# Performance work log

Measured on AMD Instinct MI355X. Metric: run time of the kernel, lower is better.

## Reference

```python
import jax, jax.numpy as jnp
import numpy as np

B, S, H = 1, 2048, 2880
NH, NKV, HD = 64, 8, 64
WIN = 128
ROPE_BASE = 10000.0


def setup_inputs() -> dict:
    key = jax.random.key(0)
    ks = jax.random.split(key, 8)

    def lin(k, fi, fo):
        return (jax.random.normal(k, (fi, fo), jnp.float32) / np.sqrt(fi)).astype(jnp.float32)

    hidden_states = jax.random.normal(ks[0], (B, S, H), jnp.float32)
    Wq = lin(ks[1], H, NH * HD)
    Wk = lin(ks[2], H, NKV * HD)
    Wv = lin(ks[3], H, NKV * HD)
    Wo = lin(ks[4], NH * HD, H)
    bq = jnp.zeros((NH * HD,), jnp.float32)
    bk = jnp.zeros((NKV * HD,), jnp.float32)
    bv = jnp.zeros((NKV * HD,), jnp.float32)
    bo = jnp.zeros((H,), jnp.float32)
    sinks = jax.random.normal(ks[5], (NH,), jnp.float32) * 0.5

    # RoPE tables, shape [B, S, HD] (rotate_half convention: halves duplicated)
    pos = jnp.arange(S, dtype=jnp.float32)
    inv_freq = 1.0 / (ROPE_BASE ** (jnp.arange(0, HD, 2, dtype=jnp.float32) / HD))
    freqs = pos[:, None] * inv_freq[None, :]          # [S, HD/2]
    emb = jnp.concatenate([freqs, freqs], axis=-1)    # [S, HD]
    cos = jnp.broadcast_to(jnp.cos(emb)[None], (B, S, HD))
    sin = jnp.broadcast_to(jnp.sin(emb)[None], (B, S, HD))

    return dict(hidden_states=hidden_states, cos=cos, sin=sin,
                Wq=Wq, bq=bq, Wk=Wk, bk=bk, Wv=Wv, bv=bv, Wo=Wo, bo=bo,
                sinks=sinks, window=WIN)


def _rotate_half(x):
    x1, x2 = jnp.split(x, 2, axis=-1)
    return jnp.concatenate([-x2, x1], axis=-1)


def reference(hidden_states, cos, sin, Wq, bq, Wk, bk, Wv, bv, Wo, bo, sinks, window):
    b, s, _ = hidden_states.shape
    nh = sinks.shape[0]
    hd = Wq.shape[1] // nh
    nkv = Wk.shape[1] // hd
    scale = hd ** -0.5

    q = (hidden_states @ Wq + bq).reshape(b, s, nh, hd)
    k = (hidden_states @ Wk + bk).reshape(b, s, nkv, hd)
    v = (hidden_states @ Wv + bv).reshape(b, s, nkv, hd)

    c = cos[:, :, None, :]  # [b, s, 1, hd]
    sn = sin[:, :, None, :]
    q = q * c + _rotate_half(q) * sn
    k = k * c + _rotate_half(k) * sn

    # GQA: expand kv heads to query heads
    g = nh // nkv
    k_rep = jnp.repeat(k, g, axis=2)  # [b, s, nh, hd]
    v_rep = jnp.repeat(v, g, axis=2)

    scores = jnp.einsum('bqhd,bkhd->bhqk', q, k_rep) * scale  # [b, nh, s, s]

    # causal sliding-window mask
    qi = jnp.arange(s)[:, None]
    ki = jnp.arange(s)[None, :]
    allowed = (qi >= ki) & (qi - ki < window)
    neg = jnp.finfo(scores.dtype).min
    scores = jnp.where(allowed[None, None], scores, neg)

    # virtual sink column at kv index s: score replaced by learned per-head bias
    sink_col = jnp.broadcast_to(sinks[None, :, None, None], (b, nh, s, 1))
    scores = jnp.concatenate([scores, sink_col], axis=-1)  # [b, nh, s, s+1]

    probs = jax.nn.softmax(scores, axis=-1)
    # sink value vector is zeros, so only real columns contribute
    out = jnp.einsum('bhqk,bkhd->bqhd', probs[..., :s], v_rep)
    out = out.reshape(b, s, nh * hd) @ Wo + bo
    return out
```

## Files before the change

### kernel.cpp

```cpp
#include <hip/hip_runtime.h>
#include <stdint.h>
#include <stddef.h>

typedef unsigned short u16;
typedef unsigned int u32;
typedef float f32x4 __attribute__((ext_vector_type(4)));
typedef __bf16 bf16x8 __attribute__((ext_vector_type(8)));
typedef uint32_t u32x4 __attribute__((ext_vector_type(4)));
typedef uint32_t u32x2 __attribute__((ext_vector_type(2)));

#define DEVINL static __device__ __forceinline__
#define VMW(n) asm volatile("s_waitcnt vmcnt(" #n ")" ::: "memory")
#define LGK0() asm volatile("s_waitcnt lgkmcnt(0)" ::: "memory")
#define SB0() __builtin_amdgcn_sched_barrier(0)

DEVINL u16 f2bf(float f) {
  union { float f; u32 u; } x; x.f = f;
  u32 r = (x.u + 0x7fffu + ((x.u >> 16) & 1u)) >> 16;
  return (u16)r;
}
DEVINL float bflo(u32 x) { union { u32 u; float f; } t; t.u = x << 16; return t.f; }
DEVINL float bfhi(u32 x) { union { u32 u; float f; } t; t.u = x & 0xffff0000u; return t.f; }

DEVINL void gl_lds16(const u16* g, u16* l) {
  __builtin_amdgcn_global_load_lds(
      (const __attribute__((address_space(1))) u32*)(const void*)g,
      (__attribute__((address_space(3))) u32*)(void*)l, 16, 0, 0);
}

DEVINL f32x4 mfma16(bf16x8 a, bf16x8 b, f32x4 c) {
  return __builtin_amdgcn_mfma_f32_16x16x32_bf16(a, b, c, 0, 0, 0);
}

DEVINL void rope8(u32x4& v1, u32x4& v2, const float* pc, const float* ps) {
  f32x4 c0 = *(const f32x4*)pc, c1 = *(const f32x4*)(pc + 4);
  f32x4 s0 = *(const f32x4*)ps, s1 = *(const f32x4*)(ps + 4);
  float C[8] = {c0[0], c0[1], c0[2], c0[3], c1[0], c1[1], c1[2], c1[3]};
  float Sn[8] = {s0[0], s0[1], s0[2], s0[3], s1[0], s1[1], s1[2], s1[3]};
  u32x4 r1, r2;
#pragma unroll
  for (int i = 0; i < 4; ++i) {
    float x1l = bflo(v1[i]), x1h = bfhi(v1[i]);
    float x2l = bflo(v2[i]), x2h = bfhi(v2[i]);
    float o1l = x1l * C[2 * i] - x2l * Sn[2 * i];
    float o1h = x1h * C[2 * i + 1] - x2h * Sn[2 * i + 1];
    float o2l = x2l * C[2 * i] + x1l * Sn[2 * i];
    float o2h = x2h * C[2 * i + 1] + x1h * Sn[2 * i + 1];
    r1[i] = (u32)f2bf(o1l) | ((u32)f2bf(o1h) << 16);
    r2[i] = (u32)f2bf(o2l) | ((u32)f2bf(o2h) << 16);
  }
  v1 = r1; v2 = r2;
}

__global__ __launch_bounds__(256) void k_pre(
    const float* __restrict__ hs, u16* __restrict__ hsb,
    const float* __restrict__ Wq, const float* __restrict__ Wk,
    const float* __restrict__ Wv, const float* __restrict__ Wo,
    u16* __restrict__ WqkvT, u16* __restrict__ WoT)
{
  __shared__ float t[64][65];
  int id = blockIdx.x;
  const int tid = threadIdx.x;
  if (id < 5760) {
    int i = id * 256 + tid;
    f32x4 v = ((const f32x4*)hs)[i];
    u32x2 o;
    o[0] = (u32)f2bf(v[0]) | ((u32)f2bf(v[1]) << 16);
    o[1] = (u32)f2bf(v[2]) | ((u32)f2bf(v[3]) << 16);
    ((u32x2*)hsb)[i] = o;
    return;
  }
  id -= 5760;
  const float* src; u16* dst; int R, C, bx, by;
  if (id < 2880)       { src = Wq; dst = WqkvT;                         R = 2880; C = 4096; bx = id & 63; by = id >> 6; }
  else if (id < 3240)  { id -= 2880; src = Wk; dst = WqkvT + (size_t)4096 * 2880; R = 2880; C = 512;  bx = id & 7;  by = id >> 3; }
  else if (id < 3600)  { id -= 3240; src = Wv; dst = WqkvT + (size_t)4608 * 2880; R = 2880; C = 512;  bx = id & 7;  by = id >> 3; }
  else                 { id -= 3600; src = Wo; dst = WoT;               R = 4096; C = 2880; bx = id % 45; by = id / 45; }
  const int r0 = by * 64, c0 = bx * 64;
  {
    const int rr = tid >> 2, cg = (tid & 3) * 16;
    const float* s = src + (size_t)(r0 + rr) * C + c0 + cg;
#pragma unroll
    for (int i = 0; i < 4; ++i) {
      f32x4 v = *(const f32x4*)(s + 4 * i);
      t[rr][cg + 4 * i + 0] = v[0];
      t[rr][cg + 4 * i + 1] = v[1];
      t[rr][cg + 4 * i + 2] = v[2];
      t[rr][cg + 4 * i + 3] = v[3];
    }
  }
  __syncthreads();
  {
    const int rg = tid & 7, cb = tid >> 3;
#pragma unroll
    for (int it = 0; it < 2; ++it) {
      const int c = cb + it * 32;
      float v[8];
#pragma unroll
      for (int i = 0; i < 8; ++i) v[i] = t[rg * 8 + i][c];
      u32x4 o;
#pragma unroll
      for (int j = 0; j < 4; ++j)
        o[j] = (u32)f2bf(v[2 * j]) | ((u32)f2bf(v[2 * j + 1]) << 16);
      *(u32x4*)(dst + (size_t)(c0 + c) * R + r0 + rg * 8) = o;
    }
  }
}

__global__ __launch_bounds__(256, 2) void k_gemmq(
    const u16* __restrict__ A, const u16* __restrict__ Bgl, u16* __restrict__ Cout,
    const float* __restrict__ pb0, const float* __restrict__ pb1, const float* __restrict__ pb2)
{
  constexpr int K = 2880, NT = 45, LDC = 5120;
  __shared__ u16 Asm[2][128 * 64];
  __shared__ u16 Bsm[2][160 * 64];

  const int bid = blockIdx.x;
  const int swz = (bid & 7) * 64 + (bid >> 3);
  const int bx = swz >> 4, by = swz & 15;
  const int m0 = by * 128, n0 = bx * 160;

  const int tid = threadIdx.x;
  const int w = tid >> 6, lane = tid & 63;
  const int l15 = lane & 15, lg = lane >> 4;
  const int wr = w >> 1, wc = w & 1;

  const u16* Ag = A + (size_t)m0 * K;
  const u16* Bg = Bgl + (size_t)n0 * K;

  auto ld1 = [&](const u16* s, u16* d, int slot) {
    int row = slot >> 3, c = slot & 7;
    gl_lds16(s + (size_t)row * K + ((c ^ (row & 7)) << 3), d + row * 64 + c * 8);
  };
  auto stApart = [&](int tg, int part) {
    u16* d = Asm[tg & 1];
    const u16* s = Ag + tg * 64;
    ld1(s, d, part * 256 + tid);
    ld1(s, d, part * 256 + 512 + tid);
  };
  auto stBa = [&](int tg) {
    u16* d = Bsm[tg & 1];
    const u16* s = Bg + tg * 64;
    ld1(s, d, tid);
    ld1(s, d, 640 + tid);
  };
  auto stBb = [&](int tg) {
    u16* d = Bsm[tg & 1];
    const u16* s = Bg + tg * 64;
    ld1(s, d, 256 + tid);
    ld1(s, d, (tid < 128) ? (512 + tid) : (768 + tid));
    ld1(s, d, 1024 + tid);
  };

  const int ra = wr * 64 + l15;
  const int rb = wc * 80 + l15;
  const int x0 = (lg ^ (l15 & 7)) << 3;
  const int x1 = x0 ^ 32;

  f32x4 acc[4][5] = {};
  bf16x8 af[2][2], bfr[5][2];

  stBa(0); stBb(0); stApart(0, 0); stApart(0, 1);
  VMW(2);
  __builtin_amdgcn_s_barrier();
  SB0();

  for (int t = 0; t < NT; ++t) {
    const u16* Ab = Asm[t & 1];
    const u16* Bb_ = Bsm[t & 1];
    const bool st = (t + 1 < NT);
#pragma unroll
    for (int m = 0; m < 2; ++m) {
      af[m][0] = *(const bf16x8*)&Ab[(ra + m * 16) * 64 + x0];
      af[m][1] = *(const bf16x8*)&Ab[(ra + m * 16) * 64 + x1];
    }
#pragma unroll
    for (int n = 0; n < 2; ++n) {
      bfr[n][0] = *(const bf16x8*)&Bb_[(rb + n * 16) * 64 + x0];
      bfr[n][1] = *(const bf16x8*)&Bb_[(rb + n * 16) * 64 + x1];
    }
    if (st) stBa(t + 1);
    LGK0(); SB0();
    __builtin_amdgcn_s_setprio(1);
#pragma unroll
    for (int kk = 0; kk < 2; ++kk)
#pragma unroll
      for (int m = 0; m < 2; ++m)
#pragma unroll
        for (int n = 0; n < 2; ++n)
          acc[m][n] = mfma16(af[m][kk], bfr[n][kk], acc[m][n]);
    __builtin_amdgcn_s_setprio(0);
#pragma unroll
    for (int n = 2; n < 5; ++n) {
      bfr[n][0] = *(const bf16x8*)&Bb_[(rb + n * 16) * 64 + x0];
      bfr[n][1] = *(const bf16x8*)&Bb_[(rb + n * 16) * 64 + x1];
    }
    if (st) stBb(t + 1);
    LGK0(); SB0();
    __builtin_amdgcn_s_setprio(1);
#pragma unroll
    for (int kk = 0; kk < 2; ++kk)
#pragma unroll
      for (int m = 0; m < 2; ++m)
#pragma unroll
        for (int n = 2; n < 5; ++n)
          acc[m][n] = mfma16(af[m][kk], bfr[n][kk], acc[m][n]);
    __builtin_amdgcn_s_setprio(0);
    if (st) { VMW(5); } else { VMW(0); }
    __builtin_amdgcn_s_barrier();
    SB0();
#pragma unroll
    for (int m = 0; m < 2; ++m) {
      af[m][0] = *(const bf16x8*)&Ab[(ra + 32 + m * 16) * 64 + x0];
      af[m][1] = *(const bf16x8*)&Ab[(ra + 32 + m * 16) * 64 + x1];
    }
    if (st) stApart(t + 1, 0);
    LGK0(); SB0();
    __builtin_amdgcn_s_setprio(1);
#pragma unroll
    for (int kk = 0; kk < 2; ++kk)
#pragma unroll
      for (int m = 0; m < 2; ++m)
#pragma unroll
        for (int n = 0; n < 2; ++n)
          acc[2 + m][n] = mfma16(af[m][kk], bfr[n][kk], acc[2 + m][n]);
    __builtin_amdgcn_s_setprio(0);
    if (st) stApart(t + 1, 1);
    __builtin_amdgcn_s_setprio(1);
#pragma unroll
    for (int kk = 0; kk < 2; ++kk)
#pragma unroll
      for (int m = 0; m < 2; ++m)
#pragma unroll
        for (int n = 2; n < 5; ++n)
          acc[2 + m][n] = mfma16(af[m][kk], bfr[n][kk], acc[2 + m][n]);
    __builtin_amdgcn_s_setprio(0);
    VMW(2);
    __builtin_amdgcn_s_barrier();
    SB0();
  }

#pragma unroll
  for (int m2 = 0; m2 < 4; ++m2)
#pragma unroll
    for (int n = 0; n < 5; ++n) {
      int col = n0 + wc * 80 + n * 16 + l15;
      float bias = (col < 4096) ? pb0[col] : (col < 4608) ? pb1[col - 4096] : pb2[col - 4608];
#pragma unroll
      for (int q = 0; q < 4; ++q) {
        int row = m0 + wr * 64 + m2 * 16 + lg * 4 + q;
        Cout[(size_t)row * LDC + col] = f2bf(acc[m2][n][q] + bias);
      }
    }
}

__global__ __launch_bounds__(256, 2) void k_gemmo(
    const u16* __restrict__ A, const u16* __restrict__ Bgl, float* __restrict__ Cout,
    const float* __restrict__ pb0)
{
  constexpr int K = 4096, NT = 64, LDC = 2880;
  __shared__ u16 Asm[2][128 * 64];
  __shared__ u16 Bsm[2][96 * 64];

  const int bid = blockIdx.x;
  const int swz = (bid & 7) * 60 + (bid >> 3);
  const int bx = swz / 16, by = swz & 15;
  const int m0 = by * 128, n0 = bx * 96;

  const int tid = threadIdx.x;
  const int w = tid >> 6, lane = tid & 63;
  const int l15 = lane & 15, lg = lane >> 4;
  const int wr = w >> 1, wc = w & 1;

  const u16* Ag = A + (size_t)m0 * K;
  const u16* Bg = Bgl + (size_t)n0 * K;

  auto ld1 = [&](const u16* s, u16* d, int slot) {
    int row = slot >> 3, c = slot & 7;
    gl_lds16(s + (size_t)row * K + ((c ^ (row & 7)) << 3), d + row * 64 + c * 8);
  };
  auto stApart = [&](int tg, int part) {
    u16* d = Asm[tg & 1];
    const u16* s = Ag + tg * 64;
    ld1(s, d, part * 256 + tid);
    ld1(s, d, part * 256 + 512 + tid);
  };
  auto stB = [&](int tg) {
    u16* d = Bsm[tg & 1];
    const u16* s = Bg + tg * 64;
    ld1(s, d, tid);
    ld1(s, d, 256 + tid);
    ld1(s, d, 512 + tid);
  };

  const int ra = wr * 64 + l15;
  const int rb = wc * 48 + l15;
  const int x0 = (lg ^ (l15 & 7)) << 3;
  const int x1 = x0 ^ 32;

  f32x4 acc[4][3] = {};
  bf16x8 af[2][2], bfr[3][2];

  stB(0); stApart(0, 0); stApart(0, 1);
  VMW(2);
  __builtin_amdgcn_s_barrier();
  SB0();

  for (int t = 0; t < NT; ++t) {
    const u16* Ab = Asm[t & 1];
    const u16* Bb_ = Bsm[t & 1];
    const bool st = (t + 1 < NT);
#pragma unroll
    for (int m = 0; m < 2; ++m) {
      af[m][0] = *(const bf16x8*)&Ab[(ra + m * 16) * 64 + x0];
      af[m][1] = *(const bf16x8*)&Ab[(ra + m * 16) * 64 + x1];
    }
#pragma unroll
    for (int n = 0; n < 3; ++n) {
      bfr[n][0] = *(const bf16x8*)&Bb_[(rb + n * 16) * 64 + x0];
      bfr[n][1] = *(const bf16x8*)&Bb_[(rb + n * 16) * 64 + x1];
    }
    if (st) { stB(t + 1); stApart(t + 1, 0); }
    LGK0(); SB0();
    __builtin_amdgcn_s_setprio(1);
#pragma unroll
    for (int kk = 0; kk < 2; ++kk)
#pragma unroll
      for (int m = 0; m < 2; ++m)
#pragma unroll
        for (int n = 0; n < 3; ++n)
          acc[m][n] = mfma16(af[m][kk], bfr[n][kk], acc[m][n]);
    __builtin_amdgcn_s_setprio(0);
    if (st) { VMW(5); } else { VMW(0); }
    __builtin_amdgcn_s_barrier();
    SB0();
#pragma unroll
    for (int m = 0; m < 2; ++m) {
      af[m][0] = *(const bf16x8*)&Ab[(ra + 32 + m * 16) * 64 + x0];
      af[m][1] = *(const bf16x8*)&Ab[(ra + 32 + m * 16) * 64 + x1];
    }
    if (st) stApart(t + 1, 1);
    LGK0(); SB0();
    __builtin_amdgcn_s_setprio(1);
#pragma unroll
    for (int kk = 0; kk < 2; ++kk)
#pragma unroll
      for (int m = 0; m < 2; ++m)
#pragma unroll
        for (int n = 0; n < 3; ++n)
          acc[2 + m][n] = mfma16(af[m][kk], bfr[n][kk], acc[2 + m][n]);
    __builtin_amdgcn_s_setprio(0);
    VMW(2);
    __builtin_amdgcn_s_barrier();
    SB0();
  }

#pragma unroll
  for (int m2 = 0; m2 < 4; ++m2)
#pragma unroll
    for (int n = 0; n < 3; ++n) {
      int col = n0 + wc * 48 + n * 16 + l15;
      float bias = pb0[col];
#pragma unroll
      for (int q = 0; q < 4; ++q) {
        int row = m0 + wr * 64 + m2 * 16 + lg * 4 + q;
        Cout[(size_t)row * LDC + col] = acc[m2][n][q] + bias;
      }
    }
}

__global__ __launch_bounds__(512, 1) void k_attn(
    const u16* __restrict__ qkv, const float* __restrict__ sinks,
    const float* __restrict__ cosb, const float* __restrict__ sinb,
    u16* __restrict__ aout)
{
  __shared__ u16 Kl[192 * 64];
  __shared__ u16 Vt[64 * 200];
  __shared__ u16 Pl[8][2][16][40];

  const int qt = blockIdx.x * 64;
  const int kv = blockIdx.y;
  const int tid = threadIdx.x;
  const int w = tid >> 6, lane = tid & 63;
  const int l15 = lane & 15, lg = lane >> 4;

  for (int idx = tid; idx < 192 * 4; idx += 512) {
    int row = idx >> 2, ch = idx & 3;
    int key = qt - 128 + row;
    u32x4 v1 = {0, 0, 0, 0}, v2 = {0, 0, 0, 0};
    if (key >= 0) {
      const u16* p = qkv + (size_t)key * 5120 + 4096 + kv * 64 + ch * 8;
      v1 = *(const u32x4*)p;
      v2 = *(const u32x4*)(p + 32);
      rope8(v1, v2, cosb + (size_t)key * 64 + ch * 8, sinb + (size_t)key * 64 + ch * 8);
    }
    int sw = (row & 7) << 4;
    *(u32x4*)((char*)Kl + row * 128 + ((ch * 16) ^ sw)) = v1;
    *(u32x4*)((char*)Kl + row * 128 + (((ch + 4) * 16) ^ sw)) = v2;
  }
  for (int idx = tid; idx < 192 * 8; idx += 512) {
    int row = idx >> 3, ch = idx & 7;
    int key = qt - 128 + row;
    u32x4 val = {0, 0, 0, 0};
    if (key >= 0) val = *(const u32x4*)(qkv + (size_t)key * 5120 + 4608 + kv * 64 + ch * 8);
    const u16* pv16 = (const u16*)&val;
#pragma unroll
    for (int j = 0; j < 8; ++j) Vt[(ch * 8 + j) * 200 + row] = pv16[j];
  }
  __syncthreads();

  const int h = kv * 8 + w;
  const float sink = sinks[h];

  for (int qs = 0; qs < 2; ++qs) {
    const int qb = qt + qs * 32;
    bf16x8 qf[2][2];
#pragma unroll
    for (int rt = 0; rt < 2; ++rt) {
      const int qrow = qb + rt * 16 + l15;
      const u16* p = qkv + (size_t)qrow * 5120 + h * 64 + lg * 8;
      union { u32x4 u; bf16x8 v; } a, b;
      a.u = *(const u32x4*)p;
      b.u = *(const u32x4*)(p + 32);
      rope8(a.u, b.u, cosb + (size_t)qrow * 64 + lg * 8, sinb + (size_t)qrow * 64 + lg * 8);
      qf[rt][0] = a.v;
      qf[rt][1] = b.v;
    }

    f32x4 S[2][5][2];
#pragma unroll
    for (int kb = 0; kb < 5; ++kb)
#pragma unroll
      for (int hh = 0; hh < 2; ++hh) {
        int krow = qs * 32 + kb * 32 + hh * 16 + l15;
        int sw = (krow & 7) << 4;
        bf16x8 kf0 = *(const bf16x8*)((const char*)Kl + krow * 128 + ((lg * 16) ^ sw));
        bf16x8 kf1 = *(const bf16x8*)((const char*)Kl + krow * 128 + ((64 + lg * 16) ^ sw));
#pragma unroll
        for (int rt = 0; rt < 2; ++rt) {
          f32x4 a = {0.f, 0.f, 0.f, 0.f};
          a = mfma16(qf[rt][0], kf0, a);
          a = mfma16(qf[rt][1], kf1, a);
          S[rt][kb][hh] = a;
        }
      }

    float inv_s[2][4];
#pragma unroll
    for (int rt = 0; rt < 2; ++rt)
#pragma unroll
      for (int r = 0; r < 4; ++r) {
        int q_abs = qb + rt * 16 + lg * 4 + r;
        float m = -1e30f;
#pragma unroll
        for (int kb = 0; kb < 5; ++kb)
#pragma unroll
          for (int hh = 0; hh < 2; ++hh) {
            int k_abs = qb - 128 + kb * 32 + hh * 16 + l15;
            float v = S[rt][kb][hh][r] * 0.125f;
            bool ok = (k_abs >= 0) && (k_abs <= q_abs) && (q_abs - k_abs < 128);
            v = ok ? v : -1e30f;
            S[rt][kb][hh][r] = v;
            m = fmaxf(m, v);
          }
        m = fmaxf(m, __shfl_xor(m, 1, 64));
        m = fmaxf(m, __shfl_xor(m, 2, 64));
        m = fmaxf(m, __shfl_xor(m, 4, 64));
        m = fmaxf(m, __shfl_xor(m, 8, 64));
        m = fmaxf(m, sink);
        float sum = 0.f;
#pragma unroll
        for (int kb = 0; kb < 5; ++kb)
#pragma unroll
          for (int hh = 0; hh < 2; ++hh) {
            float p = __expf(S[rt][kb][hh][r] - m);
            S[rt][kb][hh][r] = p;
            sum += p;
          }
        sum += __shfl_xor(sum, 1, 64);
        sum += __shfl_xor(sum, 2, 64);
        sum += __shfl_xor(sum, 4, 64);
        sum += __shfl_xor(sum, 8, 64);
        inv_s[rt][r] = 1.0f / (sum + __expf(sink - m));
      }

    f32x4 pv[2][4] = {};
#pragma unroll
    for (int kb = 0; kb < 5; ++kb) {
      asm volatile("s_waitcnt lgkmcnt(0)" ::: "memory");
#pragma unroll
      for (int rt = 0; rt < 2; ++rt)
#pragma unroll
        for (int hh = 0; hh < 2; ++hh)
#pragma unroll
          for (int r = 0; r < 4; ++r)
            Pl[w][rt][lg * 4 + r][hh * 16 + l15] = f2bf(S[rt][kb][hh][r] * inv_s[rt][r]);
      asm volatile("s_waitcnt lgkmcnt(0)" ::: "memory");
      __builtin_amdgcn_sched_barrier(0);
      bf16x8 a0 = *(const bf16x8*)&Pl[w][0][l15][lg * 8];
      bf16x8 a1 = *(const bf16x8*)&Pl[w][1][l15][lg * 8];
#pragma unroll
      for (int nt = 0; nt < 4; ++nt) {
        bf16x8 vf = *(const bf16x8*)&Vt[(nt * 16 + l15) * 200 + qs * 32 + kb * 32 + lg * 8];
        pv[0][nt] = mfma16(a0, vf, pv[0][nt]);
        pv[1][nt] = mfma16(a1, vf, pv[1][nt]);
      }
    }

#pragma unroll
    for (int rt = 0; rt < 2; ++rt)
#pragma unroll
      for (int nt = 0; nt < 4; ++nt)
#pragma unroll
        for (int r = 0; r < 4; ++r)
          aout[(size_t)(qb + rt * 16 + lg * 4 + r) * 4096 + h * 64 + nt * 16 + l15] =
              f2bf(pv[rt][nt][r]);
  }
}

extern "C" void kernel_launch(void* const* d_in, const int* in_sizes, int n_in,
                              void* d_out, int out_size, void* d_ws, size_t ws_size,
                              hipStream_t stream) {
  const float* hs    = (const float*)d_in[0];
  const float* cosb  = (const float*)d_in[1];
  const float* sinb  = (const float*)d_in[2];
  const float* Wq    = (const float*)d_in[3];
  const float* bq    = (const float*)d_in[4];
  const float* Wk    = (const float*)d_in[5];
  const float* bk    = (const float*)d_in[6];
  const float* Wv    = (const float*)d_in[7];
  const float* bv    = (const float*)d_in[8];
  const float* Wo    = (const float*)d_in[9];
  const float* bo    = (const float*)d_in[10];
  const float* sinks = (const float*)d_in[11];

  char* ws = (char*)d_ws;
  u16* hsb   = (u16*)ws;  ws += (size_t)2048 * 2880 * 2;
  u16* WqkvT = (u16*)ws;  ws += (size_t)5120 * 2880 * 2;
  u16* WoT   = (u16*)ws;  ws += (size_t)2880 * 4096 * 2;
  u16* QKV   = (u16*)ws;  ws += (size_t)2048 * 5120 * 2;
  u16* AOut  = (u16*)ws;  ws += (size_t)2048 * 4096 * 2;

  k_pre<<<12240, 256, 0, stream>>>(hs, hsb, Wq, Wk, Wv, Wo, WqkvT, WoT);

  k_gemmq<<<512, 256, 0, stream>>>(hsb, WqkvT, QKV, bq, bk, bv);

  k_attn<<<dim3(32, 8), 512, 0, stream>>>(QKV, sinks, cosb, sinb, AOut);

  k_gemmo<<<480, 256, 0, stream>>>(AOut, WoT, (float*)d_out, bo);
}
```

Measured before the change: 167.8 us.

## Fuse Wo fp32-to-bf16 transpose into output GEMM B-tile loading

Removes the separate Wo transpose/convert pass from the preprocessing kernel. The output GEMM now reads Wo directly in fp32 through registers, converts it to bf16 and writes it transposed into LDS, with the pipeline restructured to prefetch the next tile at the top of each iteration. This saves a full write and re-read of the bf16 weight copy, at the cost of strided scalar fp32 global loads and extra register and VALU work inside the GEMM. The attention grid is also flattened and its block order swizzled to improve cache locality.

```diff
diff --git a/kernel.cpp b/kernel.cpp
--- a/kernel.cpp
+++ b/kernel.cpp
@@ -55,8 +55,7 @@
 __global__ __launch_bounds__(256) void k_pre(
     const float* __restrict__ hs, u16* __restrict__ hsb,
     const float* __restrict__ Wq, const float* __restrict__ Wk,
-    const float* __restrict__ Wv, const float* __restrict__ Wo,
-    u16* __restrict__ WqkvT, u16* __restrict__ WoT)
+    const float* __restrict__ Wv, u16* __restrict__ WqkvT)
 {
   __shared__ float t[64][65];
   int id = blockIdx.x;
@@ -72,10 +71,9 @@
   }
   id -= 5760;
   const float* src; u16* dst; int R, C, bx, by;
-  if (id < 2880)       { src = Wq; dst = WqkvT;                         R = 2880; C = 4096; bx = id & 63; by = id >> 6; }
-  else if (id < 3240)  { id -= 2880; src = Wk; dst = WqkvT + (size_t)4096 * 2880; R = 2880; C = 512;  bx = id & 7;  by = id >> 3; }
-  else if (id < 3600)  { id -= 3240; src = Wv; dst = WqkvT + (size_t)4608 * 2880; R = 2880; C = 512;  bx = id & 7;  by = id >> 3; }
-  else                 { id -= 3600; src = Wo; dst = WoT;               R = 4096; C = 2880; bx = id % 45; by = id / 45; }
+  if (id < 2880)       { src = Wq; dst = WqkvT;                               R = 2880; C = 4096; bx = id & 63; by = id >> 6; }
+  else if (id < 3240)  { id -= 2880; src = Wk; dst = WqkvT + (size_t)4096 * 2880; R = 2880; C = 512; bx = id & 7; by = id >> 3; }
+  else                 { id -= 3240; src = Wv; dst = WqkvT + (size_t)4608 * 2880; R = 2880; C = 512; bx = id & 7; by = id >> 3; }
   const int r0 = by * 64, c0 = bx * 64;
   {
     const int rr = tid >> 2, cg = (tid & 3) * 16;
@@ -255,10 +253,10 @@
 }
 
 __global__ __launch_bounds__(256, 2) void k_gemmo(
-    const u16* __restrict__ A, const u16* __restrict__ Bgl, float* __restrict__ Cout,
+    const u16* __restrict__ A, const float* __restrict__ Wo, float* __restrict__ Cout,
     const float* __restrict__ pb0)
 {
-  constexpr int K = 4096, NT = 64, LDC = 2880;
+  constexpr int K = 4096, NT = 64, LDC = 2880, NW = 2880;
   __shared__ u16 Asm[2][128 * 64];
   __shared__ u16 Bsm[2][96 * 64];
 
@@ -273,7 +271,6 @@
   const int wr = w >> 1, wc = w & 1;
 
   const u16* Ag = A + (size_t)m0 * K;
-  const u16* Bg = Bgl + (size_t)n0 * K;
 
   auto ld1 = [&](const u16* s, u16* d, int slot) {
     int row = slot >> 3, c = slot & 7;
@@ -285,12 +282,35 @@
     ld1(s, d, part * 256 + tid);
     ld1(s, d, part * 256 + 512 + tid);
   };
-  auto stB = [&](int tg) {
-    u16* d = Bsm[tg & 1];
-    const u16* s = Bg + tg * 64;
-    ld1(s, d, tid);
-    ld1(s, d, 256 + tid);
-    ld1(s, d, 512 + tid);
+
+  int n_[3], oct_[3], bwoff[3];
+  const float* bp[3];
+#pragma unroll
+  for (int i = 0; i < 3; ++i) {
+    int u = i * 256 + tid;
+    n_[i] = u % 96;
+    oct_[i] = u / 96;
+    bp[i] = Wo + (size_t)oct_[i] * 8 * NW + n0 + n_[i];
+    bwoff[i] = n_[i] * 64 + ((oct_[i] ^ (n_[i] & 7)) << 3);
+  }
+  float rB[3][8];
+  auto loadB = [&](int tg) {
+#pragma unroll
+    for (int i = 0; i < 3; ++i) {
+      const float* p = bp[i] + (size_t)tg * 64 * NW;
+#pragma unroll
+      for (int j = 0; j < 8; ++j) rB[i][j] = p[(size_t)j * NW];
+    }
+  };
+  auto writeB = [&](int buf) {
+#pragma unroll
+    for (int i = 0; i < 3; ++i) {
+      u32x4 o;
+#pragma unroll
+      for (int q = 0; q < 4; ++q)
+        o[q] = (u32)f2bf(rB[i][2 * q]) | ((u32)f2bf(rB[i][2 * q + 1]) << 16);
+      *(u32x4*)(&Bsm[buf][bwoff[i]]) = o;
+    }
   };
 
   const int ra = wr * 64 + l15;
@@ -301,8 +321,12 @@
   f32x4 acc[4][3] = {};
   bf16x8 af[2][2], bfr[3][2];
 
-  stB(0); stApart(0, 0); stApart(0, 1);
-  VMW(2);
+  loadB(0);
+  stApart(0, 0); stApart(0, 1);
+  VMW(4);
+  writeB(0);
+  VMW(0);
+  LGK0();
   __builtin_amdgcn_s_barrier();
   SB0();
 
@@ -310,6 +334,11 @@
     const u16* Ab = Asm[t & 1];
     const u16* Bb_ = Bsm[t & 1];
     const bool st = (t + 1 < NT);
+    if (st) {
+      loadB(t + 1);
+      stApart(t + 1, 0); stApart(t + 1, 1);
+    }
+    SB0();
 #pragma unroll
     for (int m = 0; m < 2; ++m) {
       af[m][0] = *(const bf16x8*)&Ab[(ra + m * 16) * 64 + x0];
@@ -320,7 +349,6 @@
       bfr[n][0] = *(const bf16x8*)&Bb_[(rb + n * 16) * 64 + x0];
       bfr[n][1] = *(const bf16x8*)&Bb_[(rb + n * 16) * 64 + x1];
     }
-    if (st) { stB(t + 1); stApart(t + 1, 0); }
     LGK0(); SB0();
     __builtin_amdgcn_s_setprio(1);
 #pragma unroll
@@ -331,15 +359,11 @@
         for (int n = 0; n < 3; ++n)
           acc[m][n] = mfma16(af[m][kk], bfr[n][kk], acc[m][n]);
     __builtin_amdgcn_s_setprio(0);
-    if (st) { VMW(5); } else { VMW(0); }
-    __builtin_amdgcn_s_barrier();
-    SB0();
 #pragma unroll
     for (int m = 0; m < 2; ++m) {
       af[m][0] = *(const bf16x8*)&Ab[(ra + 32 + m * 16) * 64 + x0];
       af[m][1] = *(const bf16x8*)&Ab[(ra + 32 + m * 16) * 64 + x1];
     }
-    if (st) stApart(t + 1, 1);
     LGK0(); SB0();
     __builtin_amdgcn_s_setprio(1);
 #pragma unroll
@@ -350,7 +374,12 @@
         for (int n = 0; n < 3; ++n)
           acc[2 + m][n] = mfma16(af[m][kk], bfr[n][kk], acc[2 + m][n]);
     __builtin_amdgcn_s_setprio(0);
-    VMW(2);
+    if (st) {
+      VMW(4);
+      writeB((t + 1) & 1);
+      VMW(0);
+      LGK0();
+    }
     __builtin_amdgcn_s_barrier();
     SB0();
   }
@@ -378,8 +407,10 @@
   __shared__ u16 Vt[64 * 200];
   __shared__ u16 Pl[8][2][16][40];
 
-  const int qt = blockIdx.x * 64;
-  const int kv = blockIdx.y;
+  const int bid = blockIdx.x;
+  const int swzb = (bid & 7) * 32 + (bid >> 3);
+  const int qt = (swzb & 31) * 64;
+  const int kv = swzb >> 5;
   const int tid = threadIdx.x;
   const int w = tid >> 6, lane = tid & 63;
   const int l15 = lane & 15, lg = lane >> 4;
@@ -537,15 +568,14 @@
   char* ws = (char*)d_ws;
   u16* hsb   = (u16*)ws;  ws += (size_t)2048 * 2880 * 2;
   u16* WqkvT = (u16*)ws;  ws += (size_t)5120 * 2880 * 2;
-  u16* WoT   = (u16*)ws;  ws += (size_t)2880 * 4096 * 2;
   u16* QKV   = (u16*)ws;  ws += (size_t)2048 * 5120 * 2;
   u16* AOut  = (u16*)ws;  ws += (size_t)2048 * 4096 * 2;
 
-  k_pre<<<12240, 256, 0, stream>>>(hs, hsb, Wq, Wk, Wv, Wo, WqkvT, WoT);
+  k_pre<<<9360, 256, 0, stream>>>(hs, hsb, Wq, Wk, Wv, WqkvT);
 
   k_gemmq<<<512, 256, 0, stream>>>(hsb, WqkvT, QKV, bq, bk, bv);
 
-  k_attn<<<dim3(32, 8), 512, 0, stream>>>(QKV, sinks, cosb, sinb, AOut);
-
-  k_gemmo<<<480, 256, 0, stream>>>(AOut, WoT, (float*)d_out, bo);
-}
+  k_attn<<<256, 512, 0, stream>>>(QKV, sinks, cosb, sinb, AOut);
+
+  k_gemmo<<<480, 256, 0, stream>>>(AOut, Wo, (float*)d_out, bo);
+}
```

Result: slower. 197.7 us (+17.8%).
